# Kernel tuning notes

Measured on AMD Instinct MI355X. Metric: run time of the kernel, lower is better.

Reference implementation:

```python
import jax, jax.numpy as jnp
import numpy as np

K = 3  # kernel_size
P = K // 2


def setup_inputs() -> dict:
    key = jax.random.key(0)
    k1, k2 = jax.random.split(key)
    x = jax.random.normal(k1, (8, 64, 256, 256), dtype=jnp.float32)
    alpha = jnp.full((1, 64, 1, 1), 0.1, dtype=jnp.float32)
    return {"x": x, "alpha": alpha}


def reference(x, alpha):
    # Equivalent to F.unfold(x, K, padding=P) -> abs-diff from center -> sum over K*K -> residual.
    b, c, h, w = x.shape
    xp = jnp.pad(x, ((0, 0), (0, 0), (P, P), (P, P)))  # zero padding, same as F.unfold
    diff_sum = jnp.zeros_like(x)
    for di in range(K):
        for dj in range(K):
            neighbor = xp[:, :, di:di + h, dj:dj + w]
            diff_sum = diff_sum + jnp.abs(x - neighbor)
    return x + alpha * diff_sum
```

## Files before the change

kernel.cpp:

```cpp
#include <hip/hip_runtime.h>


constexpr int H = 256;
constexpr int W = 256;
constexpr int C = 64;

__global__ __launch_bounds__(256) void adc_kernel(
    const float* __restrict__ x,
    const float* __restrict__ alpha,
    float* __restrict__ out)
{
    const int lane = threadIdx.x & 63;
    const int wave = threadIdx.x >> 6;
    const long slab = (long)blockIdx.x;
    const long img  = slab >> 4;
    const int  s16  = (int)(slab & 15);
    const int  y0   = s16 * 16 + wave * 4;
    const int  c    = (int)(img & (C - 1));

    const float  a    = alpha[c];
    const float* imgp = x   + img * (long)(H * W);
    float*       outp = out + img * (long)(H * W);
    const int    w0   = lane * 4;

    float v[6][6];
#pragma unroll
    for (int r = 0; r < 6; ++r) {
        const int yy = y0 + r - 1;
        float4 ctr = make_float4(0.f, 0.f, 0.f, 0.f);
        if (yy >= 0 && yy < H)
            ctr = *(const float4*)(imgp + (long)yy * W + w0);
        v[r][1] = ctr.x; v[r][2] = ctr.y; v[r][3] = ctr.z; v[r][4] = ctr.w;
        const float left  = __shfl_up(ctr.w, 1);
        const float right = __shfl_down(ctr.x, 1);
        v[r][0] = (lane == 0)  ? 0.f : left;
        v[r][5] = (lane == 63) ? 0.f : right;
    }

#pragma unroll
    for (int o = 0; o < 4; ++o) {
        float4 res;
        float* rp = &res.x;
#pragma unroll
        for (int j = 0; j < 4; ++j) {
            const float xc = v[o + 1][j + 1];
            float s = 0.f;
#pragma unroll
            for (int r = 0; r < 3; ++r)
#pragma unroll
                for (int d = 0; d < 3; ++d)
                    s += fabsf(xc - v[o + r][j + d]);
            rp[j] = fmaf(a, s, xc);
        }
        *(float4*)(outp + (long)(y0 + o) * W + w0) = res;
    }
}

extern "C" void kernel_launch(void* const* d_in, const int* in_sizes, int n_in,
                              void* d_out, int out_size, void* d_ws, size_t ws_size,
                              hipStream_t stream)
{
    const float* x     = (const float*)d_in[0];
    const float* alpha = (const float*)d_in[1];
    float*       out   = (float*)d_out;

    const int grid = 8 * C * (H / 16);
    adc_kernel<<<grid, 256, 0, stream>>>(x, alpha, out);
}
```

Baseline: 234.7 us.

## Process eight rows per wave, swizzle block order, use nontemporal stores

Each wave now computes 8 output rows instead of 4, which lowers the halo re-read overhead from 6/4 to 10/8 rows per output row. All row loads are issued up front before the shuffles so more loads are in flight. The block index is swizzled across groups of 8 to spread concurrent blocks across memory. Output stores become nontemporal to avoid polluting cache, and the always-zero center term is skipped. In exchange there is higher register pressure and half as many blocks.

After: 245.4 us. 1.05x slower.

```diff
diff --git a/kernel.cpp b/kernel.cpp
--- a/kernel.cpp
+++ b/kernel.cpp
@@ -4,6 +4,8 @@
 constexpr int H = 256;
 constexpr int W = 256;
 constexpr int C = 64;
+
+typedef float vfloat4 __attribute__((ext_vector_type(4)));
 
 __global__ __launch_bounds__(256) void adc_kernel(
     const float* __restrict__ x,
@@ -12,35 +14,41 @@
 {
     const int lane = threadIdx.x & 63;
     const int wave = threadIdx.x >> 6;
-    const long slab = (long)blockIdx.x;
-    const long img  = slab >> 4;
-    const int  s16  = (int)(slab & 15);
-    const int  y0   = s16 * 16 + wave * 4;
-    const int  c    = (int)(img & (C - 1));
+
+    const int b    = blockIdx.x;
+    const int work = (b & 7) * 512 + (b >> 3);
+    const long img = work >> 3;
+    const int  s8  = work & 7;
+    const int  y0  = s8 * 32 + wave * 8;
+    const int  c   = (int)(img & (C - 1));
 
     const float  a    = alpha[c];
     const float* imgp = x   + img * (long)(H * W);
     float*       outp = out + img * (long)(H * W);
     const int    w0   = lane * 4;
 
-    float v[6][6];
+    float4 cr[10];
 #pragma unroll
-    for (int r = 0; r < 6; ++r) {
+    for (int r = 0; r < 10; ++r) {
         const int yy = y0 + r - 1;
-        float4 ctr = make_float4(0.f, 0.f, 0.f, 0.f);
+        cr[r] = make_float4(0.f, 0.f, 0.f, 0.f);
         if (yy >= 0 && yy < H)
-            ctr = *(const float4*)(imgp + (long)yy * W + w0);
-        v[r][1] = ctr.x; v[r][2] = ctr.y; v[r][3] = ctr.z; v[r][4] = ctr.w;
-        const float left  = __shfl_up(ctr.w, 1);
-        const float right = __shfl_down(ctr.x, 1);
+            cr[r] = *(const float4*)(imgp + (long)yy * W + w0);
+    }
+
+    float v[10][6];
+#pragma unroll
+    for (int r = 0; r < 10; ++r) {
+        v[r][1] = cr[r].x; v[r][2] = cr[r].y; v[r][3] = cr[r].z; v[r][4] = cr[r].w;
+        const float left  = __shfl_up(cr[r].w, 1);
+        const float right = __shfl_down(cr[r].x, 1);
         v[r][0] = (lane == 0)  ? 0.f : left;
         v[r][5] = (lane == 63) ? 0.f : right;
     }
 
 #pragma unroll
-    for (int o = 0; o < 4; ++o) {
-        float4 res;
-        float* rp = &res.x;
+    for (int o = 0; o < 8; ++o) {
+        vfloat4 res;
 #pragma unroll
         for (int j = 0; j < 4; ++j) {
             const float xc = v[o + 1][j + 1];
@@ -49,10 +57,11 @@
             for (int r = 0; r < 3; ++r)
 #pragma unroll
                 for (int d = 0; d < 3; ++d)
-                    s += fabsf(xc - v[o + r][j + d]);
-            rp[j] = fmaf(a, s, xc);
+                    if (!(r == 1 && d == 1))
+                        s += fabsf(xc - v[o + r][j + d]);
+            res[j] = fmaf(a, s, xc);
         }
-        *(float4*)(outp + (long)(y0 + o) * W + w0) = res;
+        __builtin_nontemporal_store(res, (vfloat4*)(outp + (long)(y0 + o) * W + w0));
     }
 }
 
@@ -64,6 +73,6 @@
     const float* alpha = (const float*)d_in[1];
     float*       out   = (float*)d_out;
 
-    const int grid = 8 * C * (H / 16);
+    const int grid = 8 * C * (H / 32);
     adc_kernel<<<grid, 256, 0, stream>>>(x, alpha, out);
 }
```
